# Kernel tuning notes

Measured on AMD Instinct MI355X. Metric: run time of the kernel, lower is better.

The kernel has to match this reference:

```python
import jax, jax.numpy as jnp
import numpy as np

N_NODES = 200000
N_EDGES = 3200000
N_ATTACK = 1000000
N_DEPLOY = 500000
N_MOVES = 32768

PARAM_SPECS = dict(
    g1_wl=(15, 10), g1_wr=(15, 10), g1_att=(10,), g1_b=(10,),
    g2_wl=(25, 10), g2_wr=(25, 10), g2_att=(10,), g2_b=(10,),
    g3_wl=(25, 10), g3_wr=(25, 10), g3_att=(10,), g3_b=(10,),
    lin_w=(29, 15), lin_b=(15,),
    lin2_w=(15, 1), lin2_b=(1,),
    aaa_w=(48, 20), aaa_b=(20,),
    bbb_w=(20, 1), bbb_b=(1,),
    ccc_w=(23, 20), ccc_b=(20,),
    ddd_w=(20, 1), ddd_b=(1,),
)

def _glorot(key, shape):
    lim = (6.0 / (shape[0] + shape[-1])) ** 0.5
    return jax.random.uniform(key, shape, jnp.float32, -lim, lim)

def setup_inputs() -> dict:
    key = jax.random.key(0)
    ks = jax.random.split(key, 40)
    inp = {}
    inp['x1'] = jax.random.uniform(ks[0], (N_NODES, 15), jnp.float32)
    inp['x2'] = jax.random.normal(ks[1], (4,), jnp.float32)
    inp['edges'] = jax.random.randint(ks[2], (2, N_EDGES), 0, N_NODES)
    inp['attack_src'] = jax.random.randint(ks[3], (N_ATTACK,), 0, N_NODES)
    inp['attack_dst'] = jax.random.randint(ks[4], (N_ATTACK,), 0, N_NODES)
    inp['attack_armies'] = jax.random.uniform(ks[5], (N_ATTACK,), jnp.float32) * 10.0
    inp['attack_move'] = jax.random.randint(ks[6], (N_ATTACK,), 0, N_MOVES)
    inp['deploy_target'] = jax.random.randint(ks[7], (N_DEPLOY,), 0, N_NODES)
    inp['deploy_armies'] = jax.random.uniform(ks[8], (N_DEPLOY,), jnp.float32) * 10.0
    inp['deploy_move'] = jax.random.randint(ks[9], (N_DEPLOY,), 0, N_MOVES)
    inp['num_moves'] = N_MOVES
    k = 10
    for name, shp in PARAM_SPECS.items():
        if name.endswith('_b'):
            inp[name] = jnp.zeros(shp, jnp.float32)
        else:
            inp[name] = _glorot(ks[k], shp)
            k += 1
    return inp

def _gatv2(x, src, dst, wl, wr, att, b):
    # PyG GATv2Conv, heads=1, add_self_loops=True, negative_slope=0.2, eval mode (no dropout)
    n = x.shape[0]
    xl = x @ wl  # [N, 10] (source/message transform)
    xr = x @ wr  # [N, 10] (target transform)
    loop = jnp.arange(n, dtype=src.dtype)
    s = jnp.concatenate([src, loop])
    d = jnp.concatenate([dst, loop])
    e = jax.nn.leaky_relu(xl[s] + xr[d], 0.2) @ att  # [E+N]
    m = jax.ops.segment_max(e, d, num_segments=n)
    w = jnp.exp(e - m[d])
    alpha = w / jax.ops.segment_sum(w, d, num_segments=n)[d]
    return jax.ops.segment_sum(alpha[:, None] * xl[s], d, num_segments=n) + b

def reference(x1, x2, edges, attack_src, attack_dst, attack_armies, attack_move,
              deploy_target, deploy_armies, deploy_move, num_moves,
              g1_wl, g1_wr, g1_att, g1_b, g2_wl, g2_wr, g2_att, g2_b,
              g3_wl, g3_wr, g3_att, g3_b, lin_w, lin_b, lin2_w, lin2_b,
              aaa_w, aaa_b, bbb_w, bbb_b, ccc_w, ccc_b, ddd_w, ddd_b):
    src, dst = edges[0], edges[1]
    h = jax.nn.relu(_gatv2(x1, src, dst, g1_wl, g1_wr, g1_att, g1_b))
    h = jax.nn.relu(_gatv2(jnp.concatenate([h, x1], axis=1), src, dst, g2_wl, g2_wr, g2_att, g2_b))
    h = jax.nn.relu(_gatv2(jnp.concatenate([h, x1], axis=1), src, dst, g3_wl, g3_wr, g3_att, g3_b))
    # batched attack/transfer order scoring (gather -> tiny MLP -> scatter into p)
    extra = (0.6 * attack_armies - 0.7 * (x1[attack_dst, 3] + x1[attack_dst, 4]))[:, None]
    feat_a = jnp.concatenate([h[attack_src], h[attack_dst], x1[attack_src, 3:],
                              x1[attack_dst, 1:], attack_armies[:, None], extra], axis=1)  # [Ma, 48]
    s_a = (jax.nn.relu(feat_a @ aaa_w + aaa_b) @ bbb_w + bbb_b)[:, 0]
    # batched deploy order scoring
    feat_d = jnp.concatenate([h[deploy_target], x1[deploy_target, 3:],
                              deploy_armies[:, None]], axis=1)  # [Md, 23]
    s_d = (jax.nn.relu(feat_d @ ccc_w + ccc_b) @ ddd_w + ddd_b)[:, 0]
    p = (jax.ops.segment_sum(s_a, attack_move, num_segments=num_moves)
         + jax.ops.segment_sum(s_d, deploy_move, num_segments=num_moves))
    # value head
    x2t = jnp.tile(x2, (x1.shape[0], 1))
    v = jax.nn.relu(jnp.concatenate([h, x1, x2t], axis=1) @ lin_w + lin_b) @ lin2_w + lin2_b
    V = jnp.tanh(jnp.mean(v))
    return V, jax.nn.log_softmax(p)
```

## Files before the change

kernel.cpp:

```cpp
#include <hip/hip_runtime.h>
#include <hip/hip_bf16.h>

#define HS 12
#define XLU 8
#define USU 16
#define NPART 8
#define N_CAP 200000
#define M_CAP 32768
#define E_CAP 3200000
#define BKS 10
#define CHUNK 6144

__device__ __align__(32) unsigned g_xlbA[(size_t)N_CAP * XLU];
__device__ __align__(32) unsigned g_xlbB[(size_t)N_CAP * XLU];
__device__ __align__(16) float    g_xrA[(size_t)N_CAP * HS];
__device__ __align__(16) float    g_xrB[(size_t)N_CAP * HS];
__device__ __align__(16) float    g_h [(size_t)N_CAP * HS];
__device__ __align__(64) unsigned g_us[(size_t)N_CAP * USU];
__device__ __align__(64) unsigned g_ud[(size_t)N_CAP * USU];
__device__ __align__(64) unsigned g_ut[(size_t)N_CAP * USU];
__device__ int      g_cnt[N_CAP];
__device__ int      g_off[N_CAP];
__device__ int      g_bcnt[256];
__device__ int      g_boff[256];
__device__ int      g_bcur[256];
__device__ unsigned g_staged[E_CAP];
__device__ int      g_csrc[E_CAP];
__device__ __align__(64) float g_pp[NPART][M_CAP];
__device__ float    g_p[M_CAP];
__device__ float    g_vsum[1];

__device__ __forceinline__ unsigned* xlb_buf(int s) { return s ? g_xlbB : g_xlbA; }
__device__ __forceinline__ float*    xr_buf(int s)  { return s ? g_xrB : g_xrA; }

__device__ __forceinline__ void load_row10(const float* row, float* v) {
    const float4* r4 = (const float4*)row;
    float4 a = r4[0], b = r4[1];
    float2 c = ((const float2*)row)[4];
    v[0] = a.x; v[1] = a.y; v[2] = a.z; v[3] = a.w;
    v[4] = b.x; v[5] = b.y; v[6] = b.z; v[7] = b.w;
    v[8] = c.x; v[9] = c.y;
}
__device__ __forceinline__ unsigned pack_bf2(float a, float b) {
    unsigned ua = __float_as_uint(a); ua = (ua + 0x7fffu + ((ua >> 16) & 1u)) >> 16;
    unsigned ub = __float_as_uint(b); ub = (ub + 0x7fffu + ((ub >> 16) & 1u)) >> 16;
    return ua | (ub << 16);
}
__device__ __forceinline__ void unpack_bf2(unsigned u, float& a, float& b) {
    a = __uint_as_float(u << 16);
    b = __uint_as_float(u & 0xffff0000u);
}
__device__ __forceinline__ void load_xlb(const unsigned* row, float* v) {
    uint4 q = ((const uint4*)row)[0];
    unsigned q4 = row[4];
    unpack_bf2(q.x, v[0], v[1]); unpack_bf2(q.y, v[2], v[3]);
    unpack_bf2(q.z, v[4], v[5]); unpack_bf2(q.w, v[6], v[7]);
    unpack_bf2(q4, v[8], v[9]);
}
__device__ __forceinline__ void store_xlb(unsigned* row, const float* v) {
    ((uint4*)row)[0] = make_uint4(pack_bf2(v[0], v[1]), pack_bf2(v[2], v[3]),
                                  pack_bf2(v[4], v[5]), pack_bf2(v[6], v[7]));
    row[4] = pack_bf2(v[8], v[9]);
}
__device__ __forceinline__ void load_row20_bf(const unsigned* row, float* v) {
    const uint4* r4 = (const uint4*)row;
    uint4 q0 = r4[0], q1 = r4[1], q2 = r4[2];
    unpack_bf2(q0.x, v[0], v[1]);   unpack_bf2(q0.y, v[2], v[3]);
    unpack_bf2(q0.z, v[4], v[5]);   unpack_bf2(q0.w, v[6], v[7]);
    unpack_bf2(q1.x, v[8], v[9]);   unpack_bf2(q1.y, v[10], v[11]);
    unpack_bf2(q1.z, v[12], v[13]); unpack_bf2(q1.w, v[14], v[15]);
    unpack_bf2(q2.x, v[16], v[17]); unpack_bf2(q2.y, v[18], v[19]);
}
__device__ __forceinline__ void store_row20_bf(unsigned* row, const float* v) {
    uint4* r4 = (uint4*)row;
    r4[0] = make_uint4(pack_bf2(v[0], v[1]), pack_bf2(v[2], v[3]),
                       pack_bf2(v[4], v[5]), pack_bf2(v[6], v[7]));
    r4[1] = make_uint4(pack_bf2(v[8], v[9]), pack_bf2(v[10], v[11]),
                       pack_bf2(v[12], v[13]), pack_bf2(v[14], v[15]));
    r4[2] = make_uint4(pack_bf2(v[16], v[17]), pack_bf2(v[18], v[19]), 0u, 0u);
    r4[3] = make_uint4(0u, 0u, 0u, 0u);
}

__device__ __forceinline__ void gather_core(int n, int sub, const unsigned* xlb,
                                            const float* xr_arr, const float* satt,
                                            const float* sb, float* hout) {
    float xr[10];
    load_row10(&xr_arr[(size_t)n * HS], xr);
    float m = -1e30f, den = 0.f, num[10];
#pragma unroll
    for (int j = 0; j < 10; j++) num[j] = 0.f;
    if (sub == 0) {
        float xls[10];
        load_xlb(&xlb[(size_t)n * XLU], xls);
        float acc = 0.f;
#pragma unroll
        for (int k = 0; k < 10; k++) {
            float v = xls[k] + xr[k];
            v = (v > 0.f) ? v : 0.2f * v;
            acc += v * satt[k];
            num[k] = xls[k];
        }
        m = acc;
        den = 1.f;
    }
    int lo = g_off[n], hi = lo + g_cnt[n];
    for (int e = lo + sub; e < hi; e += 4) {
        int s = g_csrc[e];
        float xls[10];
        load_xlb(&xlb[(size_t)s * XLU], xls);
        float acc = 0.f;
#pragma unroll
        for (int k = 0; k < 10; k++) {
            float v = xls[k] + xr[k];
            v = (v > 0.f) ? v : 0.2f * v;
            acc += v * satt[k];
        }
        if (acc > m) {
            float sc = __expf(m - acc);
            den *= sc;
#pragma unroll
            for (int j = 0; j < 10; j++) num[j] *= sc;
            m = acc;
        }
        float w = __expf(acc - m);
        den += w;
#pragma unroll
        for (int j = 0; j < 10; j++) num[j] += w * xls[j];
    }
#pragma unroll
    for (int off = 1; off <= 2; off <<= 1) {
        float m2 = __shfl_xor(m, off);
        float d2 = __shfl_xor(den, off);
        float M = fmaxf(m, m2);
        float s1 = __expf(m - M), s2 = __expf(m2 - M);
        den = den * s1 + d2 * s2;
#pragma unroll
        for (int j = 0; j < 10; j++) {
            float n2 = __shfl_xor(num[j], off);
            num[j] = num[j] * s1 + n2 * s2;
        }
        m = M;
    }
    float inv = 1.f / den;
#pragma unroll
    for (int j = 0; j < 10; j++) {
        float v = num[j] * inv + sb[j];
        hout[j] = (v > 0.f) ? v : 0.f;
    }
}

__global__ void k_init(int M) {
    int i = blockIdx.x * blockDim.x + threadIdx.x;
    int tot = NPART * M;
    if (i < tot) ((float*)g_pp)[i] = 0.f;
    if (i < 256) g_bcnt[i] = 0;
    if (i == tot) g_vsum[0] = 0.f;
}

__global__ void k_bhist(const int* __restrict__ dst, int E) {
    __shared__ int hist[256];
    hist[threadIdx.x] = 0;
    __syncthreads();
    for (int e = blockIdx.x * blockDim.x + threadIdx.x; e < E; e += gridDim.x * blockDim.x)
        atomicAdd(&hist[dst[e] >> BKS], 1);
    __syncthreads();
    int v = hist[threadIdx.x];
    if (v) atomicAdd(&g_bcnt[threadIdx.x], v);
}
__global__ void k_bscan() {
    __shared__ int s[256];
    int t = threadIdx.x;
    int v = g_bcnt[t];
    s[t] = v;
    __syncthreads();
    for (int d = 1; d < 256; d <<= 1) {
        int x = (t >= d) ? s[t - d] : 0;
        __syncthreads();
        s[t] += x;
        __syncthreads();
    }
    g_boff[t] = s[t] - v;
    g_bcur[t] = s[t] - v;
}
__global__ void k_bscatter(const int* __restrict__ src, const int* __restrict__ dst, int E) {
    __shared__ int hist[256], cur[256];
    int lo = blockIdx.x * CHUNK;
    int hi = lo + CHUNK; if (hi > E) hi = E;
    int tid = threadIdx.x;
    hist[tid] = 0;
    __syncthreads();
    for (int e = lo + tid; e < hi; e += 256) atomicAdd(&hist[dst[e] >> BKS], 1);
    __syncthreads();
    int h = hist[tid];
    cur[tid] = h ? atomicAdd(&g_bcur[tid], h) : 0;
    __syncthreads();
    for (int e = lo + tid; e < hi; e += 256) {
        int d = dst[e];
        int pos = atomicAdd(&cur[d >> BKS], 1);
        g_staged[pos] = ((unsigned)src[e] << BKS) | (unsigned)(d & ((1 << BKS) - 1));
    }
}
__global__ void k_bgroup(int N, int E, int nbk) {
    __shared__ int cnt[1024], offl[1024], ssum[512];
    int b = blockIdx.x;
    int nodebase = b << BKS;
    int bstart = g_boff[b];
    int bend = (b + 1 < nbk) ? g_boff[b + 1] : E;
    int tid = threadIdx.x;
    cnt[tid] = 0; cnt[tid + 512] = 0;
    __syncthreads();
    for (int e = bstart + tid; e < bend; e += 512)
        atomicAdd(&cnt[g_staged[e] & 1023u], 1);
    __syncthreads();
    int s0 = cnt[2 * tid], s1 = cnt[2 * tid + 1];
    int tsum = s0 + s1;
    ssum[tid] = tsum;
    __syncthreads();
    for (int d = 1; d < 512; d <<= 1) {
        int x = (tid >= d) ? ssum[tid - d] : 0;
        __syncthreads();
        ssum[tid] += x;
        __syncthreads();
    }
    int base = ssum[tid] - tsum;
    offl[2 * tid] = base;
    offl[2 * tid + 1] = base + s0;
    __syncthreads();
    int n0 = nodebase + 2 * tid, n1 = n0 + 1;
    if (n0 < N) { g_off[n0] = bstart + offl[2 * tid]; g_cnt[n0] = s0; }
    if (n1 < N) { g_off[n1] = bstart + offl[2 * tid + 1]; g_cnt[n1] = s1; }
    cnt[2 * tid] = offl[2 * tid];
    cnt[2 * tid + 1] = offl[2 * tid + 1];
    __syncthreads();
    for (int e = bstart + tid; e < bend; e += 512) {
        unsigned w = g_staged[e];
        int p = atomicAdd(&cnt[w & 1023u], 1);
        g_csrc[bstart + p] = (int)(w >> BKS);
    }
}

__global__ void k_pre1(const float* __restrict__ x1,
                       const float* __restrict__ wl, const float* __restrict__ wr, int N) {
    __shared__ float swl[150], swr[150];
    for (int t = threadIdx.x; t < 150; t += blockDim.x) { swl[t] = wl[t]; swr[t] = wr[t]; }
    __syncthreads();
    int n = blockIdx.x * blockDim.x + threadIdx.x;
    if (n >= N) return;
    float aL[10], aR[10];
#pragma unroll
    for (int j = 0; j < 10; j++) { aL[j] = 0.f; aR[j] = 0.f; }
    for (int k = 0; k < 15; k++) {
        float v = x1[(size_t)n * 15 + k];
#pragma unroll
        for (int j = 0; j < 10; j++) { aL[j] += v * swl[k * 10 + j]; aR[j] += v * swr[k * 10 + j]; }
    }
    store_xlb(&g_xlbA[(size_t)n * XLU], aL);
#pragma unroll
    for (int j = 0; j < 10; j++) g_xrA[(size_t)n * HS + j] = aR[j];
}

__global__ void k_gather_pre(const float* __restrict__ x1,
                             const float* __restrict__ att, const float* __restrict__ b,
                             const float* __restrict__ wl, const float* __restrict__ wr,
                             int sel_in, int N) {
    __shared__ float satt[10], sb[10], swl[250], swr[250];
    if (threadIdx.x < 10) { satt[threadIdx.x] = att[threadIdx.x]; sb[threadIdx.x] = b[threadIdx.x]; }
    for (int t = threadIdx.x; t < 250; t += blockDim.x) { swl[t] = wl[t]; swr[t] = wr[t]; }
    __syncthreads();
    int t = blockIdx.x * blockDim.x + threadIdx.x;
    int n = t >> 2, sub = t & 3;
    if (n >= N) return;
    const unsigned* xlb = xlb_buf(sel_in);
    const float* xr_arr = xr_buf(sel_in);
    unsigned* xlb_o = xlb_buf(1 - sel_in);
    float* xr_o = xr_buf(1 - sel_in);
    float h[10];
    gather_core(n, sub, xlb, xr_arr, satt, sb, h);
    if (sub == 0) {
        float aL[10], aR[10];
#pragma unroll
        for (int j = 0; j < 10; j++) { aL[j] = 0.f; aR[j] = 0.f; }
        for (int k = 0; k < 10; k++) {
            float v = h[k];
#pragma unroll
            for (int j = 0; j < 10; j++) { aL[j] += v * swl[k * 10 + j]; aR[j] += v * swr[k * 10 + j]; }
        }
        for (int k = 0; k < 15; k++) {
            float v = x1[(size_t)n * 15 + k];
#pragma unroll
            for (int j = 0; j < 10; j++) { aL[j] += v * swl[(10 + k) * 10 + j]; aR[j] += v * swr[(10 + k) * 10 + j]; }
        }
        store_xlb(&xlb_o[(size_t)n * XLU], aL);
#pragma unroll
        for (int j = 0; j < 10; j++) xr_o[(size_t)n * HS + j] = aR[j];
    }
}

__global__ void k_gather3(const float* __restrict__ att, const float* __restrict__ b,
                          int sel_in, int N) {
    __shared__ float satt[10], sb[10];
    if (threadIdx.x < 10) { satt[threadIdx.x] = att[threadIdx.x]; sb[threadIdx.x] = b[threadIdx.x]; }
    __syncthreads();
    int t = blockIdx.x * blockDim.x + threadIdx.x;
    int n = t >> 2, sub = t & 3;
    if (n >= N) return;
    float h[10];
    gather_core(n, sub, xlb_buf(sel_in), xr_buf(sel_in), satt, sb, h);
    if (sub == 0) {
#pragma unroll
        for (int j = 0; j < 10; j++) g_h[(size_t)n * HS + j] = h[j];
    }
}

__global__ void k_prep_value(const float* __restrict__ x1,
                             const float* __restrict__ aw, const float* __restrict__ cw,
                             const float* __restrict__ x2,
                             const float* __restrict__ w1, const float* __restrict__ b1,
                             const float* __restrict__ w2, const float* __restrict__ bias2,
                             int N) {
    __shared__ float sA[48 * 20], sC[23 * 20], sw1[29 * 15];
    __shared__ float sb1[15], sw2v[15], sx2[4], sb2v;
    __shared__ float red[256];
    for (int t = threadIdx.x; t < 48 * 20; t += blockDim.x) sA[t] = aw[t];
    for (int t = threadIdx.x; t < 23 * 20; t += blockDim.x) sC[t] = cw[t];
    for (int t = threadIdx.x; t < 29 * 15; t += blockDim.x) sw1[t] = w1[t];
    if (threadIdx.x < 15) { sb1[threadIdx.x] = b1[threadIdx.x]; sw2v[threadIdx.x] = w2[threadIdx.x]; }
    if (threadIdx.x < 4) sx2[threadIdx.x] = x2[threadIdx.x];
    if (threadIdx.x == 0) sb2v = bias2[0];
    __syncthreads();
    int n = blockIdx.x * blockDim.x + threadIdx.x;
    float vout = 0.f;
    if (n < N) {
        float hv[10], xv[15];
        load_row10(&g_h[(size_t)n * HS], hv);
#pragma unroll
        for (int k = 0; k < 15; k++) xv[k] = x1[(size_t)n * 15 + k];
        float us[20], ud[20], ut[20];
#pragma unroll
        for (int j = 0; j < 20; j++) { us[j] = 0.f; ud[j] = 0.f; ut[j] = 0.f; }
        for (int k = 0; k < 10; k++) {
            float h = hv[k];
#pragma unroll
            for (int j = 0; j < 20; j++) {
                us[j] += h * sA[k * 20 + j];
                ud[j] += h * sA[(10 + k) * 20 + j];
                ut[j] += h * sC[k * 20 + j];
            }
        }
        for (int k = 0; k < 12; k++) {
            float v = xv[3 + k];
#pragma unroll
            for (int j = 0; j < 20; j++) {
                us[j] += v * sA[(20 + k) * 20 + j];
                ut[j] += v * sC[(10 + k) * 20 + j];
            }
        }
        for (int k = 0; k < 14; k++) {
            float v = xv[1 + k];
#pragma unroll
            for (int j = 0; j < 20; j++) ud[j] += v * sA[(32 + k) * 20 + j];
        }
        float t34 = -0.7f * (xv[3] + xv[4]);
#pragma unroll
        for (int j = 0; j < 20; j++) ud[j] += t34 * sA[47 * 20 + j];
        store_row20_bf(&g_us[(size_t)n * USU], us);
        store_row20_bf(&g_ud[(size_t)n * USU], ud);
        store_row20_bf(&g_ut[(size_t)n * USU], ut);
        float acc[15];
#pragma unroll
        for (int j = 0; j < 15; j++) acc[j] = sb1[j];
        for (int k = 0; k < 10; k++) {
            float f = hv[k];
#pragma unroll
            for (int j = 0; j < 15; j++) acc[j] += f * sw1[k * 15 + j];
        }
        for (int k = 0; k < 15; k++) {
            float f = xv[k];
#pragma unroll
            for (int j = 0; j < 15; j++) acc[j] += f * sw1[(10 + k) * 15 + j];
        }
        for (int k = 0; k < 4; k++) {
            float f = sx2[k];
#pragma unroll
            for (int j = 0; j < 15; j++) acc[j] += f * sw1[(25 + k) * 15 + j];
        }
        vout = sb2v;
#pragma unroll
        for (int j = 0; j < 15; j++) { float r = (acc[j] > 0.f) ? acc[j] : 0.f; vout += r * sw2v[j]; }
    }
    red[threadIdx.x] = vout;
    __syncthreads();
    for (int s = 128; s > 0; s >>= 1) {
        if (threadIdx.x < (unsigned)s) red[threadIdx.x] += red[threadIdx.x + s];
        __syncthreads();
    }
    if (threadIdx.x == 0) atomicAdd(&g_vsum[0], red[0]);
}

__global__ void k_score(const int* __restrict__ asrc, const int* __restrict__ adst,
                        const float* __restrict__ aarm, const int* __restrict__ amove,
                        const float* __restrict__ aw, const float* __restrict__ ab,
                        const float* __restrict__ bw, const float* __restrict__ bb,
                        const int* __restrict__ dtar, const float* __restrict__ darm,
                        const int* __restrict__ dmove,
                        const float* __restrict__ cw, const float* __restrict__ cb,
                        const float* __restrict__ dw, const float* __restrict__ db,
                        int Ma, int Md, int na) {
    __shared__ float swa[20], sbias[20], sw2[20], sb2;
    bool isA = (blockIdx.x < (unsigned)na);
    float* pp = g_pp[blockIdx.x & (NPART - 1)];
    if (threadIdx.x < 20) {
        if (isA) {
            swa[threadIdx.x] = aw[46 * 20 + threadIdx.x] + 0.6f * aw[47 * 20 + threadIdx.x];
            sbias[threadIdx.x] = ab[threadIdx.x];
            sw2[threadIdx.x] = bw[threadIdx.x];
        } else {
            swa[threadIdx.x] = cw[22 * 20 + threadIdx.x];
            sbias[threadIdx.x] = cb[threadIdx.x];
            sw2[threadIdx.x] = dw[threadIdx.x];
        }
    }
    if (threadIdx.x == 0) sb2 = isA ? bb[0] : db[0];
    __syncthreads();
    if (isA) {
        int base = blockIdx.x * 512 + threadIdx.x;
#pragma unroll
        for (int r = 0; r < 2; r++) {
            int i = base + r * 256;
            if (i >= Ma) break;
            int s = asrc[i], d = adst[i];
            float a = aarm[i];
            float us[20], ud[20];
            load_row20_bf(&g_us[(size_t)s * USU], us);
            load_row20_bf(&g_ud[(size_t)d * USU], ud);
            float sres = sb2;
#pragma unroll
            for (int j = 0; j < 20; j++) {
                float acc = sbias[j] + us[j] + ud[j] + a * swa[j];
                float rr = (acc > 0.f) ? acc : 0.f;
                sres += rr * sw2[j];
            }
            atomicAdd(&pp[amove[i]], sres);
        }
    } else {
        int base = (blockIdx.x - na) * 512 + threadIdx.x;
#pragma unroll
        for (int r = 0; r < 2; r++) {
            int i = base + r * 256;
            if (i >= Md) break;
            int t = dtar[i];
            float a = darm[i];
            float ut[20];
            load_row20_bf(&g_ut[(size_t)t * USU], ut);
            float sres = sb2;
#pragma unroll
            for (int j = 0; j < 20; j++) {
                float acc = sbias[j] + ut[j] + a * swa[j];
                float rr = (acc > 0.f) ? acc : 0.f;
                sres += rr * sw2[j];
            }
            atomicAdd(&pp[dmove[i]], sres);
        }
    }
}

__global__ void k_final(float* __restrict__ out, int M, int N) {
    __shared__ float red[1024];
    int tid = threadIdx.x;
    float mx = -1e30f;
    for (int i = tid; i < M; i += 1024) {
        float s = 0.f;
#pragma unroll
        for (int q = 0; q < NPART; q++) s += g_pp[q][i];
        g_p[i] = s;
        mx = fmaxf(mx, s);
    }
    red[tid] = mx;
    __syncthreads();
    for (int s = 512; s > 0; s >>= 1) {
        if (tid < s) red[tid] = fmaxf(red[tid], red[tid + s]);
        __syncthreads();
    }
    float pmax = red[0];
    __syncthreads();
    float sm = 0.f;
    for (int i = tid; i < M; i += 1024) sm += __expf(g_p[i] - pmax);
    red[tid] = sm;
    __syncthreads();
    for (int s = 512; s > 0; s >>= 1) {
        if (tid < s) red[tid] += red[tid + s];
        __syncthreads();
    }
    float lse = pmax + logf(red[0]);
    if (tid == 0) out[0] = tanhf(g_vsum[0] / (float)N);
    for (int i = tid; i < M; i += 1024) out[1 + i] = g_p[i] - lse;
}

extern "C" void kernel_launch(void* const* d_in, const int* in_sizes, int n_in,
                              void* d_out, int out_size, void* d_ws, size_t ws_size,
                              hipStream_t stream) {
    const float* x1 = (const float*)d_in[0];
    const float* x2 = (const float*)d_in[1];
    const int* edges = (const int*)d_in[2];
    const int* asrc = (const int*)d_in[3];
    const int* adst = (const int*)d_in[4];
    const float* aarm = (const float*)d_in[5];
    const int* amove = (const int*)d_in[6];
    const int* dtar = (const int*)d_in[7];
    const float* darm = (const float*)d_in[8];
    const int* dmove = (const int*)d_in[9];
    const int pb = n_in - 24;
    const float* g1_wl  = (const float*)d_in[pb + 0];
    const float* g1_wr  = (const float*)d_in[pb + 1];
    const float* g1_att = (const float*)d_in[pb + 2];
    const float* g1_b   = (const float*)d_in[pb + 3];
    const float* g2_wl  = (const float*)d_in[pb + 4];
    const float* g2_wr  = (const float*)d_in[pb + 5];
    const float* g2_att = (const float*)d_in[pb + 6];
    const float* g2_b   = (const float*)d_in[pb + 7];
    const float* g3_wl  = (const float*)d_in[pb + 8];
    const float* g3_wr  = (const float*)d_in[pb + 9];
    const float* g3_att = (const float*)d_in[pb + 10];
    const float* g3_b   = (const float*)d_in[pb + 11];
    const float* lin_w  = (const float*)d_in[pb + 12];
    const float* lin_b  = (const float*)d_in[pb + 13];
    const float* lin2_w = (const float*)d_in[pb + 14];
    const float* lin2_b = (const float*)d_in[pb + 15];
    const float* aaa_w  = (const float*)d_in[pb + 16];
    const float* aaa_b  = (const float*)d_in[pb + 17];
    const float* bbb_w  = (const float*)d_in[pb + 18];
    const float* bbb_b  = (const float*)d_in[pb + 19];
    const float* ccc_w  = (const float*)d_in[pb + 20];
    const float* ccc_b  = (const float*)d_in[pb + 21];
    const float* ddd_w  = (const float*)d_in[pb + 22];
    const float* ddd_b  = (const float*)d_in[pb + 23];

    int N = in_sizes[0] / 15;
    int E = in_sizes[2] / 2;
    const int Ma = in_sizes[3];
    const int Md = in_sizes[7];
    int M = out_size - 1;
    if (N > N_CAP) N = N_CAP;
    if (E > E_CAP) E = E_CAP;
    if (M > M_CAP) M = M_CAP;
    const int* src = edges;
    const int* dst = edges + E;

    const int nb = (N + 255) / 256;
    const int nb4 = (4 * N + 255) / 256;
    const int nbk = (N + (1 << BKS) - 1) >> BKS;
    const int nsc = (E + CHUNK - 1) / CHUNK;
    const int na = (Ma + 511) / 512, nd = (Md + 511) / 512;

    k_init<<<(NPART * M + 256) / 256, 256, 0, stream>>>(M);
    k_bhist<<<512, 256, 0, stream>>>(dst, E);
    k_bscan<<<1, 256, 0, stream>>>();
    k_bscatter<<<nsc, 256, 0, stream>>>(src, dst, E);
    k_bgroup<<<nbk, 512, 0, stream>>>(N, E, nbk);

    k_pre1<<<nb, 256, 0, stream>>>(x1, g1_wl, g1_wr, N);
    k_gather_pre<<<nb4, 256, 0, stream>>>(x1, g1_att, g1_b, g2_wl, g2_wr, 0, N);
    k_gather_pre<<<nb4, 256, 0, stream>>>(x1, g2_att, g2_b, g3_wl, g3_wr, 1, N);
    k_gather3<<<nb4, 256, 0, stream>>>(g3_att, g3_b, 0, N);

    k_prep_value<<<nb, 256, 0, stream>>>(x1, aaa_w, ccc_w, x2, lin_w, lin_b, lin2_w, lin2_b, N);
    k_score<<<na + nd, 256, 0, stream>>>(asrc, adst, aarm, amove, aaa_w, aaa_b, bbb_w, bbb_b,
                                         dtar, darm, dmove, ccc_w, ccc_b, ddd_w, ddd_b,
                                         Ma, Md, na);
    k_final<<<1, 1024, 0, stream>>>((float*)d_out, M, N);
}
```

Measured before the change: 634.8 us.

## Fuse layer-3 gather with per-node projection and value head

Merges the third GATv2 aggregation kernel with the per-node precompute and value-head kernel, so the aggregated h stays in registers and the g_h buffer is no longer written and re-read. The four threads that cooperate on each node's gather now split the follow-up work: the three 20-wide projections and the value MLP each go to a different sub-lane. This removes one launch and a global round trip and spreads the per-node arithmetic across four threads, but the fused kernel now loads all the shared weight tables in every block and the four branches diverge within a wavefront.

```diff
diff --git a/kernel.cpp b/kernel.cpp
--- a/kernel.cpp
+++ b/kernel.cpp
@@ -15,7 +15,6 @@
 __device__ __align__(32) unsigned g_xlbB[(size_t)N_CAP * XLU];
 __device__ __align__(16) float    g_xrA[(size_t)N_CAP * HS];
 __device__ __align__(16) float    g_xrB[(size_t)N_CAP * HS];
-__device__ __align__(16) float    g_h [(size_t)N_CAP * HS];
 __device__ __align__(64) unsigned g_us[(size_t)N_CAP * USU];
 __device__ __align__(64) unsigned g_ud[(size_t)N_CAP * USU];
 __device__ __align__(64) unsigned g_ut[(size_t)N_CAP * USU];
@@ -296,31 +295,18 @@
     }
 }
 
-__global__ void k_gather3(const float* __restrict__ att, const float* __restrict__ b,
-                          int sel_in, int N) {
+__global__ void k_gather3_prep(const float* __restrict__ x1,
+                               const float* __restrict__ att, const float* __restrict__ b,
+                               const float* __restrict__ aw, const float* __restrict__ cw,
+                               const float* __restrict__ x2,
+                               const float* __restrict__ w1, const float* __restrict__ b1,
+                               const float* __restrict__ w2, const float* __restrict__ bias2,
+                               int sel_in, int N) {
     __shared__ float satt[10], sb[10];
-    if (threadIdx.x < 10) { satt[threadIdx.x] = att[threadIdx.x]; sb[threadIdx.x] = b[threadIdx.x]; }
-    __syncthreads();
-    int t = blockIdx.x * blockDim.x + threadIdx.x;
-    int n = t >> 2, sub = t & 3;
-    if (n >= N) return;
-    float h[10];
-    gather_core(n, sub, xlb_buf(sel_in), xr_buf(sel_in), satt, sb, h);
-    if (sub == 0) {
-#pragma unroll
-        for (int j = 0; j < 10; j++) g_h[(size_t)n * HS + j] = h[j];
-    }
-}
-
-__global__ void k_prep_value(const float* __restrict__ x1,
-                             const float* __restrict__ aw, const float* __restrict__ cw,
-                             const float* __restrict__ x2,
-                             const float* __restrict__ w1, const float* __restrict__ b1,
-                             const float* __restrict__ w2, const float* __restrict__ bias2,
-                             int N) {
     __shared__ float sA[48 * 20], sC[23 * 20], sw1[29 * 15];
     __shared__ float sb1[15], sw2v[15], sx2[4], sb2v;
     __shared__ float red[256];
+    if (threadIdx.x < 10) { satt[threadIdx.x] = att[threadIdx.x]; sb[threadIdx.x] = b[threadIdx.x]; }
     for (int t = threadIdx.x; t < 48 * 20; t += blockDim.x) sA[t] = aw[t];
     for (int t = threadIdx.x; t < 23 * 20; t += blockDim.x) sC[t] = cw[t];
     for (int t = threadIdx.x; t < 29 * 15; t += blockDim.x) sw1[t] = w1[t];
@@ -328,65 +314,86 @@
     if (threadIdx.x < 4) sx2[threadIdx.x] = x2[threadIdx.x];
     if (threadIdx.x == 0) sb2v = bias2[0];
     __syncthreads();
-    int n = blockIdx.x * blockDim.x + threadIdx.x;
+    int t = blockIdx.x * blockDim.x + threadIdx.x;
+    int n = t >> 2, sub = t & 3;
     float vout = 0.f;
     if (n < N) {
-        float hv[10], xv[15];
-        load_row10(&g_h[(size_t)n * HS], hv);
+        float h[10];
+        gather_core(n, sub, xlb_buf(sel_in), xr_buf(sel_in), satt, sb, h);
+        float xv[15];
 #pragma unroll
         for (int k = 0; k < 15; k++) xv[k] = x1[(size_t)n * 15 + k];
-        float us[20], ud[20], ut[20];
-#pragma unroll
-        for (int j = 0; j < 20; j++) { us[j] = 0.f; ud[j] = 0.f; ut[j] = 0.f; }
-        for (int k = 0; k < 10; k++) {
-            float h = hv[k];
-#pragma unroll
-            for (int j = 0; j < 20; j++) {
-                us[j] += h * sA[k * 20 + j];
-                ud[j] += h * sA[(10 + k) * 20 + j];
-                ut[j] += h * sC[k * 20 + j];
-            }
-        }
-        for (int k = 0; k < 12; k++) {
-            float v = xv[3 + k];
-#pragma unroll
-            for (int j = 0; j < 20; j++) {
-                us[j] += v * sA[(20 + k) * 20 + j];
-                ut[j] += v * sC[(10 + k) * 20 + j];
-            }
-        }
-        for (int k = 0; k < 14; k++) {
-            float v = xv[1 + k];
-#pragma unroll
-            for (int j = 0; j < 20; j++) ud[j] += v * sA[(32 + k) * 20 + j];
-        }
-        float t34 = -0.7f * (xv[3] + xv[4]);
-#pragma unroll
-        for (int j = 0; j < 20; j++) ud[j] += t34 * sA[47 * 20 + j];
-        store_row20_bf(&g_us[(size_t)n * USU], us);
-        store_row20_bf(&g_ud[(size_t)n * USU], ud);
-        store_row20_bf(&g_ut[(size_t)n * USU], ut);
-        float acc[15];
-#pragma unroll
-        for (int j = 0; j < 15; j++) acc[j] = sb1[j];
-        for (int k = 0; k < 10; k++) {
-            float f = hv[k];
-#pragma unroll
-            for (int j = 0; j < 15; j++) acc[j] += f * sw1[k * 15 + j];
-        }
-        for (int k = 0; k < 15; k++) {
-            float f = xv[k];
-#pragma unroll
-            for (int j = 0; j < 15; j++) acc[j] += f * sw1[(10 + k) * 15 + j];
-        }
-        for (int k = 0; k < 4; k++) {
-            float f = sx2[k];
-#pragma unroll
-            for (int j = 0; j < 15; j++) acc[j] += f * sw1[(25 + k) * 15 + j];
-        }
-        vout = sb2v;
-#pragma unroll
-        for (int j = 0; j < 15; j++) { float r = (acc[j] > 0.f) ? acc[j] : 0.f; vout += r * sw2v[j]; }
+        if (sub == 0) {
+            float us[20];
+#pragma unroll
+            for (int j = 0; j < 20; j++) us[j] = 0.f;
+            for (int k = 0; k < 10; k++) {
+                float hv = h[k];
+#pragma unroll
+                for (int j = 0; j < 20; j++) us[j] += hv * sA[k * 20 + j];
+            }
+            for (int k = 0; k < 12; k++) {
+                float v = xv[3 + k];
+#pragma unroll
+                for (int j = 0; j < 20; j++) us[j] += v * sA[(20 + k) * 20 + j];
+            }
+            store_row20_bf(&g_us[(size_t)n * USU], us);
+        } else if (sub == 1) {
+            float ud[20];
+#pragma unroll
+            for (int j = 0; j < 20; j++) ud[j] = 0.f;
+            for (int k = 0; k < 10; k++) {
+                float hv = h[k];
+#pragma unroll
+                for (int j = 0; j < 20; j++) ud[j] += hv * sA[(10 + k) * 20 + j];
+            }
+            for (int k = 0; k < 14; k++) {
+                float v = xv[1 + k];
+#pragma unroll
+                for (int j = 0; j < 20; j++) ud[j] += v * sA[(32 + k) * 20 + j];
+            }
+            float t34 = -0.7f * (xv[3] + xv[4]);
+#pragma unroll
+            for (int j = 0; j < 20; j++) ud[j] += t34 * sA[47 * 20 + j];
+            store_row20_bf(&g_ud[(size_t)n * USU], ud);
+        } else if (sub == 2) {
+            float ut[20];
+#pragma unroll
+            for (int j = 0; j < 20; j++) ut[j] = 0.f;
+            for (int k = 0; k < 10; k++) {
+                float hv = h[k];
+#pragma unroll
+                for (int j = 0; j < 20; j++) ut[j] += hv * sC[k * 20 + j];
+            }
+            for (int k = 0; k < 12; k++) {
+                float v = xv[3 + k];
+#pragma unroll
+                for (int j = 0; j < 20; j++) ut[j] += v * sC[(10 + k) * 20 + j];
+            }
+            store_row20_bf(&g_ut[(size_t)n * USU], ut);
+        } else {
+            float acc[15];
+#pragma unroll
+            for (int j = 0; j < 15; j++) acc[j] = sb1[j];
+            for (int k = 0; k < 10; k++) {
+                float f = h[k];
+#pragma unroll
+                for (int j = 0; j < 15; j++) acc[j] += f * sw1[k * 15 + j];
+            }
+            for (int k = 0; k < 15; k++) {
+                float f = xv[k];
+#pragma unroll
+                for (int j = 0; j < 15; j++) acc[j] += f * sw1[(10 + k) * 15 + j];
+            }
+            for (int k = 0; k < 4; k++) {
+                float f = sx2[k];
+#pragma unroll
+                for (int j = 0; j < 15; j++) acc[j] += f * sw1[(25 + k) * 15 + j];
+            }
+            vout = sb2v;
+#pragma unroll
+            for (int j = 0; j < 15; j++) { float r = (acc[j] > 0.f) ? acc[j] : 0.f; vout += r * sw2v[j]; }
+        }
     }
     red[threadIdx.x] = vout;
     __syncthreads();
@@ -561,9 +568,9 @@
     k_pre1<<<nb, 256, 0, stream>>>(x1, g1_wl, g1_wr, N);
     k_gather_pre<<<nb4, 256, 0, stream>>>(x1, g1_att, g1_b, g2_wl, g2_wr, 0, N);
     k_gather_pre<<<nb4, 256, 0, stream>>>(x1, g2_att, g2_b, g3_wl, g3_wr, 1, N);
-    k_gather3<<<nb4, 256, 0, stream>>>(g3_att, g3_b, 0, N);
-
-    k_prep_value<<<nb, 256, 0, stream>>>(x1, aaa_w, ccc_w, x2, lin_w, lin_b, lin2_w, lin2_b, N);
+    k_gather3_prep<<<nb4, 256, 0, stream>>>(x1, g3_att, g3_b, aaa_w, ccc_w, x2,
+                                            lin_w, lin_b, lin2_w, lin2_b, 0, N);
+
     k_score<<<na + nd, 256, 0, stream>>>(asrc, adst, aarm, amove, aaa_w, aaa_b, bbb_w, bbb_b,
                                          dtar, darm, dmove, ccc_w, ccc_b, ddd_w, ddd_b,
                                          Ma, Md, na);
```

Measured after the change: 630.1 us. Within noise of the previous version (-0.7%).
